# Performance work log

Hardware: AMD Instinct MI355X
Metric: run time of the kernel (lower is better)

Reference implementation:

```python
import math
import jax, jax.numpy as jnp
import numpy as np

NUM_PRE_NMS = 2000
NMS_THR = 0.7
MIN_SIZE = 16.0
LOG_MAX = math.log(1000.0 / 16)  # clamp on dh, dw as in the torch module

B, A, H, W = 8, 3, 200, 304
STRIDE = 4


def _make_anchors():
    # grid anchors, channel-last anchor ordering to match permute(0,2,3,1)
    sizes = np.array([32.0, 64.0, 128.0], dtype=np.float32)  # A sizes
    ys = (np.arange(H, dtype=np.float32) + 0.5) * STRIDE
    xs = (np.arange(W, dtype=np.float32) + 0.5) * STRIDE
    cy, cx = np.meshgrid(ys, xs, indexing="ij")  # [H,W]
    cx = cx[:, :, None]
    cy = cy[:, :, None]
    half = (sizes / 2.0)[None, None, :]  # [1,1,A]
    anc = np.stack([cx - half, cy - half, cx + half, cy + half], axis=-1)  # [H,W,A,4]
    anc = anc.reshape(-1, 4)  # [H*W*A, 4]
    anc = np.broadcast_to(anc[None], (B, anc.shape[0], 4)).copy()
    return jnp.asarray(anc)


def setup_inputs() -> dict:
    key = jax.random.key(0)
    k1, k2 = jax.random.split(key)
    cls_logits = jax.random.normal(k1, (B, A, H, W), dtype=jnp.float32)
    regs = jax.random.normal(k2, (B, 4 * A, H, W), dtype=jnp.float32) * 0.1
    anchors = _make_anchors()
    return {"cls_logits": cls_logits, "regs": regs, "anchors": anchors,
            "image_h": 800, "image_w": 1216}


def _box_iou(boxes):
    # boxes: [K,4] -> iou [K,K]
    x1, y1, x2, y2 = boxes[:, 0], boxes[:, 1], boxes[:, 2], boxes[:, 3]
    area = (x2 - x1) * (y2 - y1)
    ix1 = jnp.maximum(x1[:, None], x1[None, :])
    iy1 = jnp.maximum(y1[:, None], y1[None, :])
    ix2 = jnp.minimum(x2[:, None], x2[None, :])
    iy2 = jnp.minimum(y2[:, None], y2[None, :])
    iw = jnp.clip(ix2 - ix1, 0.0)
    ih = jnp.clip(iy2 - iy1, 0.0)
    inter = iw * ih
    union = area[:, None] + area[None, :] - inter
    return inter / jnp.maximum(union, 1e-6)


def _nms_one(boxes, valid):
    # boxes sorted by descending score; greedy suppression, fixed-size keep mask
    k = boxes.shape[0]
    iou = _box_iou(boxes)
    later = jnp.arange(k)

    def body(i, keep):
        sup = (iou[i] > NMS_THR) & keep[i] & (later > i)
        return keep & ~sup

    return jax.lax.fori_loop(0, k, body, valid)


def reference(cls_logits, regs, anchors, image_h, image_w):
    b = cls_logits.shape[0]
    # scores/regs in channel-last anchor order (matches permute(0,2,3,1))
    scores = jnp.transpose(cls_logits, (0, 2, 3, 1)).reshape(b, -1)       # [B,N]
    deltas = jnp.transpose(regs, (0, 2, 3, 1)).reshape(b, -1, 4)          # [B,N,4]
    n = scores.shape[1]
    k = min(NUM_PRE_NMS, n)

    top_scores, idx = jax.lax.top_k(scores, k)                            # [B,K]
    top_deltas = jnp.take_along_axis(deltas, idx[:, :, None], axis=1)     # [B,K,4]
    top_anchors = jnp.take_along_axis(anchors, idx[:, :, None], axis=1)   # [B,K,4]

    dx, dy = top_deltas[..., 0], top_deltas[..., 1]
    dh = jnp.minimum(top_deltas[..., 2], LOG_MAX)
    dw = jnp.minimum(top_deltas[..., 3], LOG_MAX)
    ah = top_anchors[..., 3] - top_anchors[..., 1]
    aw = top_anchors[..., 2] - top_anchors[..., 0]
    cx = aw / 2
    cy = ah / 2
    px = cx + dx * aw
    py = cy + dy * ah
    ph = jnp.exp(dh) * ah
    pw = jnp.exp(dw) * aw
    boxes = jnp.stack([px - pw / 2, py - ph / 2, px + pw / 2, py + ph / 2], axis=-1)  # [B,K,4]

    # size filter on clamped coords (as in _nms)
    w_img = jnp.float32(image_w)
    h_img = jnp.float32(image_h)
    bw = jnp.clip(boxes[..., 2], 0.0, w_img) - jnp.clip(boxes[..., 0], 0.0, w_img)
    bh = jnp.clip(boxes[..., 3], 0.0, h_img) - jnp.clip(boxes[..., 1], 0.0, h_img)
    valid = (bw >= MIN_SIZE) & (bh >= MIN_SIZE)

    keep = jax.vmap(_nms_one)(boxes, valid)                               # [B,K]
    out_boxes = boxes * keep[..., None].astype(boxes.dtype)
    return out_boxes, top_scores, keep
```

## Files before the change

### kernel.cpp

```cpp
#include <hip/hip_runtime.h>

#define HWSZ 60800
#define NA 3
#define NTOT 182400
#define KSEL 2000
#define CANDCAP 8192
#define NBATCH 8
#define GSPLIT 128
#define LOG_MAX_F 4.135166556742356f

#define OFF_H1    0
#define OFF_CCNT  65536
#define OFF_DONE  65568
#define ZR_BYTES  65600
#define OFF_SEL   65600
#define OFF_BOX   65728
#define OFF_VALID 321728
#define OFF_SUP   385728
#define OFF_CAND  385728

__device__ __forceinline__ unsigned int xform(float f) {
    unsigned int b = __float_as_uint(f);
    return b ^ ((unsigned int)((int)b >> 31) | 0x80000000u);
}

__global__ __launch_bounds__(256) void k_hist_scan(const float* __restrict__ cls,
                                                   unsigned int* __restrict__ hist1,
                                                   unsigned int* __restrict__ done,
                                                   uint4* __restrict__ selinfo) {
    int b = blockIdx.y, part = blockIdx.x, tid = threadIdx.x;
    __shared__ unsigned int h[2048];
    for (int i = tid; i < 2048; i += 256) h[i] = 0u;
    __syncthreads();
    const float4* base4 = (const float4*)(cls + (size_t)b * NTOT);
    const int n4 = NTOT / 4;
    int per = (n4 + GSPLIT - 1) / GSPLIT;
    int lo = part * per, hi = lo + per;
    if (hi > n4) hi = n4;
    for (int i = lo + tid; i < hi; i += 256) {
        float4 v = base4[i];
        atomicAdd(&h[xform(v.x) >> 21], 1u);
        atomicAdd(&h[xform(v.y) >> 21], 1u);
        atomicAdd(&h[xform(v.z) >> 21], 1u);
        atomicAdd(&h[xform(v.w) >> 21], 1u);
    }
    __syncthreads();
    unsigned int* gh = hist1 + b * 2048;
    for (int i = tid; i < 2048; i += 256)
        if (h[i]) atomicAdd(&gh[i], h[i]);

    __shared__ unsigned int slast;
    __syncthreads();
    if (tid == 0) {
        __threadfence();
        unsigned int old = __hip_atomic_fetch_add(&done[b], 1u, __ATOMIC_ACQ_REL,
                                                  __HIP_MEMORY_SCOPE_AGENT);
        slast = (old == GSPLIT - 1) ? 1u : 0u;
    }
    __syncthreads();
    if (!slast) return;

    __shared__ unsigned int sa[2048], sb[2048];
    #pragma unroll
    for (int k = 0; k < 8; ++k) {
        int i = tid + k * 256;
        sa[i] = __hip_atomic_load(&gh[i], __ATOMIC_RELAXED, __HIP_MEMORY_SCOPE_AGENT);
    }
    unsigned int* src = sa; unsigned int* dst = sb;
    for (int d = 1; d < 2048; d <<= 1) {
        __syncthreads();
        #pragma unroll
        for (int k = 0; k < 8; ++k) {
            int i = tid + k * 256;
            dst[i] = src[i] + ((i + d < 2048) ? src[i + d] : 0u);
        }
        unsigned int* t = src; src = dst; dst = t;
    }
    __syncthreads();
    #pragma unroll
    for (int k = 0; k < 8; ++k) {
        int i = tid + k * 256;
        unsigned int c = src[i];
        unsigned int cn = (i < 2047) ? src[i + 1] : 0u;
        if (c >= KSEL && cn < KSEL)
            selinfo[b] = make_uint4((unsigned int)i, cn, KSEL - cn, 0u);
    }
}

__global__ __launch_bounds__(256) void k_gather(const float* __restrict__ cls,
                                                const uint4* __restrict__ selinfo,
                                                unsigned long long* __restrict__ cand,
                                                unsigned int* __restrict__ ccnt) {
    int b = blockIdx.y, part = blockIdx.x, tid = threadIdx.x;
    unsigned int bin = selinfo[b].x;
    __shared__ unsigned long long lbuf[1024];
    __shared__ unsigned int lcnt, gbase;
    if (tid == 0) lcnt = 0u;
    __syncthreads();
    const float4* base4 = (const float4*)(cls + (size_t)b * NTOT);
    const int n4 = NTOT / 4;
    int per = (n4 + GSPLIT - 1) / GSPLIT;
    int lo = part * per, hi = lo + per;
    if (hi > n4) hi = n4;
    for (int i = lo + tid; i < hi; i += 256) {
        float4 v = base4[i];
        float vals[4] = {v.x, v.y, v.z, v.w};
        int idx0 = i * 4;
        #pragma unroll
        for (int q = 0; q < 4; ++q) {
            unsigned int u = xform(vals[q]);
            if ((u >> 21) >= bin) {
                int idx = idx0 + q;
                int a = idx / HWSZ;
                int hw = idx - a * HWSZ;
                unsigned int n = (unsigned int)(hw * NA + a);
                unsigned int pos = atomicAdd(&lcnt, 1u);
                if (pos < 1024u)
                    lbuf[pos] = ((unsigned long long)u << 32) | (unsigned long long)(~n);
            }
        }
    }
    __syncthreads();
    if (tid == 0) {
        unsigned int c = lcnt < 1024u ? lcnt : 1024u;
        gbase = atomicAdd(&ccnt[b], c);
    }
    __syncthreads();
    unsigned int c = lcnt < 1024u ? lcnt : 1024u;
    unsigned int gb = gbase;
    for (unsigned int i = tid; i < c; i += 256) {
        unsigned int p = gb + i;
        if (p < CANDCAP) cand[(size_t)b * CANDCAP + p] = lbuf[i];
    }
}

__global__ __launch_bounds__(256) void k_rank_decode(
        const unsigned long long* __restrict__ cand,
        const unsigned int* __restrict__ ccnt,
        const float* __restrict__ regs,
        const float* __restrict__ anchors,
        const int* __restrict__ img_h,
        const int* __restrict__ img_w,
        float* __restrict__ out_scores,
        float4* __restrict__ boxes_ws,
        unsigned int* __restrict__ valid_ws) {
    int b = blockIdx.y;
    int tid = threadIdx.x;
    unsigned int sc = ccnt[b];
    if (sc > CANDCAP) sc = CANDCAP;
    unsigned int kbase = blockIdx.x * 64;
    if (kbase >= sc) return;
    int ki = tid & 63;
    int q = tid >> 6;
    int lane = tid & 63;
    const unsigned long long* sb_ = cand + (size_t)b * CANDCAP;
    unsigned int r = kbase + (unsigned int)ki;
    unsigned long long mykey = (r < sc) ? sb_[r] : 0ULL;

    unsigned int qs = ((sc + 255u) >> 8) << 6;
    unsigned int lo = (unsigned int)q * qs;
    unsigned int hi = lo + qs;
    if (hi > sc) hi = sc;

    unsigned int cnt = 0u;
    for (unsigned int base = lo; base < hi; base += 64) {
        unsigned long long kj = 0ULL;
        if (base + (unsigned int)lane < hi) kj = sb_[base + lane];
        unsigned int klo = (unsigned int)kj;
        unsigned int khi = (unsigned int)(kj >> 32);
        #pragma unroll
        for (int t = 0; t < 64; ++t) {
            unsigned int lo_ = (unsigned int)__builtin_amdgcn_readlane((int)klo, t);
            unsigned int hi_ = (unsigned int)__builtin_amdgcn_readlane((int)khi, t);
            unsigned long long kt = ((unsigned long long)hi_ << 32) | (unsigned long long)lo_;
            cnt += (kt > mykey) ? 1u : 0u;
        }
    }
    __shared__ unsigned int cntsh[4][64];
    cntsh[q][ki] = cnt;
    __syncthreads();
    if (tid >= 64) return;
    unsigned int rank = cntsh[0][ki] + cntsh[1][ki] + cntsh[2][ki] + cntsh[3][ki];
    if (r >= sc || rank >= KSEL) return;

    int hv = img_h[0];
    int wv = img_w[0];
    float himg = (hv > 0 && hv < 100000) ? (float)hv : __int_as_float(hv);
    float wimg = (wv > 0 && wv < 100000) ? (float)wv : __int_as_float(wv);

    unsigned int u = (unsigned int)(mykey >> 32);
    unsigned int n = ~((unsigned int)mykey);
    unsigned int bits = (u & 0x80000000u) ? (u & 0x7FFFFFFFu) : ~u;
    float score = __uint_as_float(bits);
    int a = (int)(n % NA);
    int hw = (int)(n / NA);
    const float* rp = regs + ((size_t)b * (4 * NA) + 4 * a) * HWSZ + hw;
    float dx = rp[0 * HWSZ];
    float dy = rp[1 * HWSZ];
    float dh = rp[2 * HWSZ];
    float dw = rp[3 * HWSZ];
    const float* ap = anchors + ((size_t)b * NTOT + n) * 4;
    float ax1 = ap[0], ay1 = ap[1], ax2 = ap[2], ay2 = ap[3];
    float ahh = ay2 - ay1;
    float aww = ax2 - ax1;
    float cx = aww * 0.5f;
    float cy = ahh * 0.5f;
    float px = cx + dx * aww;
    float py = cy + dy * ahh;
    dh = fminf(dh, LOG_MAX_F);
    dw = fminf(dw, LOG_MAX_F);
    float ph = expf(dh) * ahh;
    float pw = expf(dw) * aww;
    float x1 = px - pw * 0.5f;
    float y1 = py - ph * 0.5f;
    float x2 = px + pw * 0.5f;
    float y2 = py + ph * 0.5f;
    float bwv = fminf(fmaxf(x2, 0.f), wimg) - fminf(fmaxf(x1, 0.f), wimg);
    float bhv = fminf(fmaxf(y2, 0.f), himg) - fminf(fmaxf(y1, 0.f), himg);
    unsigned int valid = (bwv >= 16.f && bhv >= 16.f) ? 1u : 0u;
    size_t o = (size_t)b * KSEL + rank;
    out_scores[o] = score;
    boxes_ws[o] = make_float4(x1, y1, x2, y2);
    valid_ws[o] = valid;
}

__global__ __launch_bounds__(256) void k_supmat(const float4* __restrict__ boxes_ws,
                                                unsigned long long* __restrict__ sup) {
    int ct = blockIdx.x;
    int rt = blockIdx.y;
    int b  = blockIdx.z;
    if (ct * 64 + 63 < rt * 256) return;
    int tid = threadIdx.x;
    __shared__ float4 colbox[64];
    int j0 = ct * 64;
    if (tid < 64) {
        int jl = j0 + tid;
        colbox[tid] = (jl < KSEL) ? boxes_ws[(size_t)b * KSEL + jl]
                                  : make_float4(0.f, 0.f, 0.f, 0.f);
    }
    __syncthreads();
    int i = rt * 256 + tid;
    if (i >= KSEL) return;
    float4 bi = boxes_ws[(size_t)b * KSEL + i];
    float area_i = (bi.z - bi.x) * (bi.w - bi.y);
    unsigned long long word = 0ULL;
    #pragma unroll 8
    for (int jj = 0; jj < 64; ++jj) {
        int j = j0 + jj;
        float4 bj = colbox[jj];
        float area_j = (bj.z - bj.x) * (bj.w - bj.y);
        float ix1 = fmaxf(bi.x, bj.x);
        float iy1 = fmaxf(bi.y, bj.y);
        float ix2 = fminf(bi.z, bj.z);
        float iy2 = fminf(bi.w, bj.w);
        float iw = fmaxf(ix2 - ix1, 0.f);
        float ih = fmaxf(iy2 - iy1, 0.f);
        float inter = iw * ih;
        float uni = area_i + area_j - inter;
        float iou = inter / fmaxf(uni, 1e-6f);
        bool s = (j > i) && (j < KSEL) && (iou > 0.7f);
        if (s) word |= (1ULL << jj);
    }
    sup[((size_t)b * KSEL + i) * 32 + ct] = word;
}

#define LOAD_TILE(wnext, buf)                                                \
    {                                                                        \
        int gbase_ = (wnext) * 2048;                                         \
        _Pragma("unroll")                                                    \
        for (int k = 0; k < 8; ++k) {                                        \
            int e_ = tid + k * 256;                                          \
            int row_ = (wnext) * 64 + (e_ >> 5);                             \
            buf[k] = (row_ < KSEL) ? srow[gbase_ + e_] : 0ULL;               \
        }                                                                    \
    }

#define PROCESS_TILE(w, buf)                                                 \
    {                                                                        \
        if (myword == (w)) {                                                 \
            _Pragma("unroll")                                                \
            for (int k = 0; k < 8; ++k)                                      \
                diag[(tid >> 5) + k * 8] = buf[k];                           \
        }                                                                    \
        __syncthreads();      \
        unsigned long long dval_ = diag[lane];                               \
        unsigned long long nz_ = __ballot(dval_ != 0ULL);                    \
        unsigned int dlo_ = (unsigned int)dval_;                             \
        unsigned int dhi_ = (unsigned int)(dval_ >> 32);                     \
        unsigned long long pend_ =                                           \
            ((unsigned long long)accw[(w) * 2 + 1] << 32)                    \
            | (unsigned long long)accw[(w) * 2];                             \
        unsigned long long c64_ = kws[w] & ~pend_;                           \
        unsigned int clo_ = __builtin_amdgcn_readfirstlane((unsigned int)c64_);        \
        unsigned int chi_ = __builtin_amdgcn_readfirstlane((unsigned int)(c64_ >> 32));\
        unsigned long long cur_ = ((unsigned long long)chi_ << 32)           \
                                  | (unsigned long long)clo_;                \
        if (cur_) {                                                          \
             \
            unsigned long long rem_ = cur_ & nz_;                            \
            while (rem_) {                                                   \
                int bit_ = __builtin_ctzll(rem_);                            \
                unsigned int lo_ = (unsigned int)__builtin_amdgcn_readlane((int)dlo_, bit_); \
                unsigned int hi_ = (unsigned int)__builtin_amdgcn_readlane((int)dhi_, bit_); \
                unsigned long long d_ = ((unsigned long long)hi_ << 32)      \
                                        | (unsigned long long)lo_;           \
                cur_ &= ~d_;                                                 \
                rem_ = cur_ & nz_ & ~((2ULL << bit_) - 1ULL);                \
            }                                                                \
            if (tid == 0) fin[w] = cur_;                                     \
            unsigned long long v_ = 0ULL;                                    \
            _Pragma("unroll")                                                \
            for (int k = 0; k < 8; ++k) {                                    \
                int row_ = (tid >> 5) + k * 8;                               \
                if ((cur_ >> row_) & 1ULL) v_ |= buf[k];                     \
            }                                                                \
            v_ |= __shfl_xor(v_, 32, 64);                                    \
            if (lane < 32 && myword > (w) && v_) {                           \
                atomicOr(&accw[myword * 2], (unsigned int)v_);               \
                atomicOr(&accw[myword * 2 + 1], (unsigned int)(v_ >> 32));   \
            }                                                                \
        } else if (tid == 0) {                                               \
            fin[w] = 0ULL;                                                   \
        }                                                                    \
    }

__global__ __launch_bounds__(256) void k_nms_scan(const unsigned long long* __restrict__ sup,
                                                  const unsigned int* __restrict__ valid_ws,
                                                  const float4* __restrict__ boxes_ws,
                                                  float* __restrict__ out_boxes,
                                                  float* __restrict__ out_keep) {
    int b = blockIdx.x;
    int tid = threadIdx.x;
    int lane = tid & 63;
    int myword = tid & 31;
    __shared__ unsigned long long kws[32];
    __shared__ unsigned long long fin[32];
    __shared__ unsigned long long diag[64];
    __shared__ unsigned int accw[64];
    const unsigned long long* srow = sup + (size_t)b * KSEL * 32;

    if (tid < 32) {
        unsigned long long kw = 0ULL;
        const uint4* vv = (const uint4*)(valid_ws + (size_t)b * KSEL);
        #pragma unroll 4
        for (int q = 0; q < 16; ++q) {
            uint4 x = vv[tid * 16 + q];
            int base = q * 4;
            if (x.x) kw |= 1ULL << (base + 0);
            if (x.y) kw |= 1ULL << (base + 1);
            if (x.z) kw |= 1ULL << (base + 2);
            if (x.w) kw |= 1ULL << (base + 3);
        }
        if (tid == 31) kw &= 0xFFFFULL;
        kws[tid] = kw;
    }
    if (tid < 64) accw[tid] = 0u;

    unsigned long long A[8], B[8];
    LOAD_TILE(0, A);
    LOAD_TILE(1, B);

    for (int t = 0; t < 16; ++t) {
        int w = 2 * t;
        PROCESS_TILE(w, A);
        if (w + 2 < 32) LOAD_TILE(w + 2, A);
        PROCESS_TILE(w + 1, B);
        if (w + 3 < 32) LOAD_TILE(w + 3, B);
    }
    __syncthreads();

    float4* ob4 = (float4*)out_boxes;
    for (int r = tid; r < KSEL; r += 256) {
        float kf = (float)((fin[r >> 6] >> (r & 63)) & 1ULL);
        size_t o = (size_t)b * KSEL + r;
        out_keep[o] = kf;
        float4 bx = boxes_ws[o];
        ob4[o] = make_float4(bx.x * kf, bx.y * kf, bx.z * kf, bx.w * kf);
    }
}

extern "C" void kernel_launch(void* const* d_in, const int* in_sizes, int n_in,
                              void* d_out, int out_size, void* d_ws, size_t ws_size,
                              hipStream_t stream) {
    const float* cls     = (const float*)d_in[0];
    const float* regs    = (const float*)d_in[1];
    const float* anchors = (const float*)d_in[2];
    const int*   img_h   = (const int*)d_in[3];
    const int*   img_w   = (const int*)d_in[4];

    float* out = (float*)d_out;
    float* out_boxes  = out;
    float* out_scores = out + 64000;
    float* out_keep   = out + 80000;

    char* ws = (char*)d_ws;
    unsigned int* hist1      = (unsigned int*)(ws + OFF_H1);
    unsigned int* ccnt       = (unsigned int*)(ws + OFF_CCNT);
    unsigned int* done       = (unsigned int*)(ws + OFF_DONE);
    uint4* selinfo           = (uint4*)(ws + OFF_SEL);
    float4* boxes_ws         = (float4*)(ws + OFF_BOX);
    unsigned int* valid_ws   = (unsigned int*)(ws + OFF_VALID);
    unsigned long long* sup  = (unsigned long long*)(ws + OFF_SUP);
    unsigned long long* cand = (unsigned long long*)(ws + OFF_CAND);

    hipMemsetAsync(ws, 0, ZR_BYTES, stream);
    k_hist_scan<<<dim3(GSPLIT, NBATCH), 256, 0, stream>>>(cls, hist1, done, selinfo);
    k_gather<<<dim3(GSPLIT, NBATCH), 256, 0, stream>>>(cls, selinfo, cand, ccnt);
    k_rank_decode<<<dim3(CANDCAP / 64, NBATCH), 256, 0, stream>>>(cand, ccnt, regs, anchors,
                                                                  img_h, img_w, out_scores,
                                                                  boxes_ws, valid_ws);
    k_supmat<<<dim3(32, 8, NBATCH), 256, 0, stream>>>(boxes_ws, sup);
    k_nms_scan<<<NBATCH, 256, 0, stream>>>(sup, valid_ws, boxes_ws, out_boxes, out_keep);
}
```

Measured before the change: 244.6 us.

## Resolve NMS diagonal blocks via transposed column masks and ballot fixed-point iteration

The supmat kernel now also writes a transposed copy of each 64x64 diagonal suppression block using ballots. The NMS scan preloads these column masks into LDS. It then resolves intra-block suppression with a ballot-based fixed-point iteration instead of a serial per-bit readlane loop. This removes the per-tile diag staging and __syncthreads and replaces them with a lighter waitcnt+barrier. The trade-off is extra transpose work in supmat, 16KB of extra LDS, and an iteration count that depends on suppression chain depth.

```diff
diff --git a/kernel.cpp b/kernel.cpp
--- a/kernel.cpp
+++ b/kernel.cpp
@@ -18,10 +18,16 @@
 #define OFF_VALID 321728
 #define OFF_SUP   385728
 #define OFF_CAND  385728
+#define OFF_SUPT  4481728
 
 __device__ __forceinline__ unsigned int xform(float f) {
     unsigned int b = __float_as_uint(f);
     return b ^ ((unsigned int)((int)b >> 31) | 0x80000000u);
+}
+
+__device__ __forceinline__ void bar_lds() {
+    asm volatile("s_waitcnt lgkmcnt(0)" ::: "memory");
+    __builtin_amdgcn_s_barrier();
 }
 
 __global__ __launch_bounds__(256) void k_hist_scan(const float* __restrict__ cls,
@@ -225,7 +231,8 @@
 }
 
 __global__ __launch_bounds__(256) void k_supmat(const float4* __restrict__ boxes_ws,
-                                                unsigned long long* __restrict__ sup) {
+                                                unsigned long long* __restrict__ sup,
+                                                unsigned long long* __restrict__ supT) {
     int ct = blockIdx.x;
     int rt = blockIdx.y;
     int b  = blockIdx.z;
@@ -262,6 +269,17 @@
         if (s) word |= (1ULL << jj);
     }
     sup[((size_t)b * KSEL + i) * 32 + ct] = word;
+
+    if (ct == rt * 4 + (tid >> 6)) {
+        int lane = tid & 63;
+        unsigned long long cm = 0ULL;
+        #pragma unroll
+        for (int j = 0; j < 64; ++j) {
+            unsigned long long t = __ballot((word >> j) & 1ULL);
+            if (lane == j) cm = t;
+        }
+        supT[((size_t)b * 32 + ct) * 64 + lane] = cm;
+    }
 }
 
 #define LOAD_TILE(wnext, buf)                                                \
@@ -277,36 +295,25 @@
 
 #define PROCESS_TILE(w, buf)                                                 \
     {                                                                        \
-        if (myword == (w)) {                                                 \
-            _Pragma("unroll")                                                \
-            for (int k = 0; k < 8; ++k)                                      \
-                diag[(tid >> 5) + k * 8] = buf[k];                           \
-        }                                                                    \
-        __syncthreads();      \
-        unsigned long long dval_ = diag[lane];                               \
-        unsigned long long nz_ = __ballot(dval_ != 0ULL);                    \
-        unsigned int dlo_ = (unsigned int)dval_;                             \
-        unsigned int dhi_ = (unsigned int)(dval_ >> 32);                     \
+        bar_lds();                                                           \
         unsigned long long pend_ =                                           \
             ((unsigned long long)accw[(w) * 2 + 1] << 32)                    \
             | (unsigned long long)accw[(w) * 2];                             \
-        unsigned long long c64_ = kws[w] & ~pend_;                           \
-        unsigned int clo_ = __builtin_amdgcn_readfirstlane((unsigned int)c64_);        \
-        unsigned int chi_ = __builtin_amdgcn_readfirstlane((unsigned int)(c64_ >> 32));\
+        unsigned long long cand_ = kws[w] & ~pend_;                          \
+        unsigned int clo_ = __builtin_amdgcn_readfirstlane((unsigned int)cand_);        \
+        unsigned int chi_ = __builtin_amdgcn_readfirstlane((unsigned int)(cand_ >> 32));\
         unsigned long long cur_ = ((unsigned long long)chi_ << 32)           \
                                   | (unsigned long long)clo_;                \
         if (cur_) {                                                          \
-             \
-            unsigned long long rem_ = cur_ & nz_;                            \
-            while (rem_) {                                                   \
-                int bit_ = __builtin_ctzll(rem_);                            \
-                unsigned int lo_ = (unsigned int)__builtin_amdgcn_readlane((int)dlo_, bit_); \
-                unsigned int hi_ = (unsigned int)__builtin_amdgcn_readlane((int)dhi_, bit_); \
-                unsigned long long d_ = ((unsigned long long)hi_ << 32)      \
-                                        | (unsigned long long)lo_;           \
-                cur_ &= ~d_;                                                 \
-                rem_ = cur_ & nz_ & ~((2ULL << bit_) - 1ULL);                \
+            unsigned long long cmw_ = colT[(w) * 64 + lane];                 \
+            unsigned long long k_ = cur_;                                    \
+            for (;;) {                                                       \
+                unsigned long long sup_ = __ballot((k_ & cmw_) != 0ULL);     \
+                unsigned long long k2_ = cur_ & ~sup_;                       \
+                if (k2_ == k_) break;                                        \
+                k_ = k2_;                                                    \
             }                                                                \
+            cur_ = k_;                                                       \
             if (tid == 0) fin[w] = cur_;                                     \
             unsigned long long v_ = 0ULL;                                    \
             _Pragma("unroll")                                                \
@@ -325,6 +332,7 @@
     }
 
 __global__ __launch_bounds__(256) void k_nms_scan(const unsigned long long* __restrict__ sup,
+                                                  const unsigned long long* __restrict__ supT,
                                                   const unsigned int* __restrict__ valid_ws,
                                                   const float4* __restrict__ boxes_ws,
                                                   float* __restrict__ out_boxes,
@@ -335,9 +343,18 @@
     int myword = tid & 31;
     __shared__ unsigned long long kws[32];
     __shared__ unsigned long long fin[32];
-    __shared__ unsigned long long diag[64];
     __shared__ unsigned int accw[64];
+    __shared__ unsigned long long colT[32 * 64];
     const unsigned long long* srow = sup + (size_t)b * KSEL * 32;
+
+    {
+        const unsigned long long* stb = supT + (size_t)b * 2048;
+        #pragma unroll
+        for (int k = 0; k < 8; ++k) {
+            int i = tid + k * 256;
+            colT[i] = stb[i];
+        }
+    }
 
     if (tid < 32) {
         unsigned long long kw = 0ULL;
@@ -367,7 +384,7 @@
         PROCESS_TILE(w + 1, B);
         if (w + 3 < 32) LOAD_TILE(w + 3, B);
     }
-    __syncthreads();
+    bar_lds();
 
     float4* ob4 = (float4*)out_boxes;
     for (int r = tid; r < KSEL; r += 256) {
@@ -402,6 +419,7 @@
     unsigned int* valid_ws   = (unsigned int*)(ws + OFF_VALID);
     unsigned long long* sup  = (unsigned long long*)(ws + OFF_SUP);
     unsigned long long* cand = (unsigned long long*)(ws + OFF_CAND);
+    unsigned long long* supT = (unsigned long long*)(ws + OFF_SUPT);
 
     hipMemsetAsync(ws, 0, ZR_BYTES, stream);
     k_hist_scan<<<dim3(GSPLIT, NBATCH), 256, 0, stream>>>(cls, hist1, done, selinfo);
@@ -409,6 +427,6 @@
     k_rank_decode<<<dim3(CANDCAP / 64, NBATCH), 256, 0, stream>>>(cand, ccnt, regs, anchors,
                                                                   img_h, img_w, out_scores,
                                                                   boxes_ws, valid_ws);
-    k_supmat<<<dim3(32, 8, NBATCH), 256, 0, stream>>>(boxes_ws, sup);
-    k_nms_scan<<<NBATCH, 256, 0, stream>>>(sup, valid_ws, boxes_ws, out_boxes, out_keep);
-}
+    k_supmat<<<dim3(32, 8, NBATCH), 256, 0, stream>>>(boxes_ws, sup, supT);
+    k_nms_scan<<<NBATCH, 256, 0, stream>>>(sup, supT, valid_ws, boxes_ws, out_boxes, out_keep);
+}
```

New measurement: 238.0 us. 1.03x faster.
